# Optimization experiments

Measured on AMD Instinct MI355X. Metric: run time of the kernel, lower is better.

Reference implementation:

```python
import jax, jax.numpy as jnp
from jax import lax
import numpy as np

B, D, P = 4096, 256, 512  # batch, encoded_space_dim (=d_prototypes), n_prototypes
BN_EPS = 1e-5  # torch BatchNorm eval with running_mean=0, running_var=1


def _conv(x, w, stride, pad):
    # x: NCHW, w: OIHW
    return lax.conv_general_dilated(x, w, (stride, stride), [(pad, pad), (pad, pad)],
                                    dimension_numbers=('NCHW', 'OIHW', 'NCHW'))


def _conv_t(x, w, stride, pad, out_pad):
    # torch ConvTranspose2d; w in torch layout [Cin, Cout, kh, kw]
    k = w.shape[2]
    wf = jnp.flip(w, (2, 3)).transpose(1, 0, 2, 3)  # -> OIHW, flipped
    lo = k - 1 - pad
    hi = k - 1 - pad + out_pad
    return lax.conv_general_dilated(x, wf, (1, 1), [(lo, hi), (lo, hi)],
                                    lhs_dilation=(stride, stride),
                                    dimension_numbers=('NCHW', 'OIHW', 'NCHW'))


def _bn(x, g, b):
    # eval-mode BatchNorm2d with running_mean=0, running_var=1
    s = g / jnp.sqrt(1.0 + BN_EPS)
    return x * s[None, :, None, None] + b[None, :, None, None]


def _bias(x, b):
    return x + b[None, :, None, None]


def setup_inputs() -> dict:
    key = jax.random.key(0)
    ks = jax.random.split(key, 32)
    n = jax.random.normal
    inp = {
        'x': jax.random.uniform(ks[0], (B, 1, 28, 28), jnp.float32),
        # encoder
        'w1': n(ks[1], (8, 1, 3, 3), jnp.float32) * 0.1, 'b1': jnp.zeros((8,), jnp.float32),
        'w2': n(ks[2], (16, 8, 3, 3), jnp.float32) * 0.1, 'b2': jnp.zeros((16,), jnp.float32),
        'g2': jnp.ones((16,), jnp.float32), 'bt2': jnp.zeros((16,), jnp.float32),
        'w3': n(ks[3], (D, 16, 3, 3), jnp.float32) * 0.1, 'b3': jnp.zeros((D,), jnp.float32),
        # prototypes (torch.rand init)
        'protolayer': jax.random.uniform(ks[4], (P, D, 1, 1), jnp.float32),
        # up layer (ConvTranspose2d(D, D, 5), torch layout [Cin,Cout,kh,kw])
        'wup': n(ks[5], (D, D, 5, 5), jnp.float32) * 0.02, 'bup': jnp.zeros((D,), jnp.float32),
        'gup': jnp.ones((D,), jnp.float32), 'btup': jnp.zeros((D,), jnp.float32),
        # decoder
        'wd1': n(ks[6], (D, 16, 3, 3), jnp.float32) * 0.05, 'bd1': jnp.zeros((16,), jnp.float32),
        'gd1': jnp.ones((16,), jnp.float32), 'btd1': jnp.zeros((16,), jnp.float32),
        'wd2': n(ks[7], (16, 8, 3, 3), jnp.float32) * 0.1, 'bd2': jnp.zeros((8,), jnp.float32),
        'gd2': jnp.ones((8,), jnp.float32), 'btd2': jnp.zeros((8,), jnp.float32),
        'wd3': n(ks[8], (8, 1, 3, 3), jnp.float32) * 0.1, 'bd3': jnp.zeros((1,), jnp.float32),
    }
    return inp


def reference(x, w1, b1, w2, b2, g2, bt2, w3, b3, protolayer,
              wup, bup, gup, btup,
              wd1, bd1, gd1, btd1, wd2, bd2, gd2, btd2, wd3, bd3):
    # ---- encoder: 28 -> 14 -> 7 -> 5 ----
    h = jax.nn.relu(_bias(_conv(x, w1, 2, 1), b1))
    h = jax.nn.relu(_bn(_bias(_conv(h, w2, 2, 1), b2), g2, bt2))
    h = jax.nn.relu(_bias(_conv(h, w3, 1, 0), b3))  # [B, D, 5, 5]

    # ---- l2 'convolution' with 1x1 prototypes ----
    p = protolayer[:, :, 0, 0]                                  # [P, D]
    x2_patch_sum = jnp.sum(h * h, axis=1)                       # ones-conv, 1x1 kernel -> channel sum [B,5,5]
    xp = jnp.einsum('bdhw,pd->bphw', h, p)                      # [B, P, 5, 5]
    p2 = jnp.sum(p * p, axis=1)                                 # [P]
    distances = jax.nn.relu(x2_patch_sum[:, None] - 2.0 * xp + p2[None, :, None, None])

    # min-pool over full spatial extent
    min_distances = jnp.min(distances, axis=(2, 3))             # [B, P]
    prototype_activations = -min_distances                      # 'linear' distance_2_similarity
    w = jax.nn.softmax(prototype_activations, axis=1)
    z = jnp.einsum('bp,pdkl->bdkl', w, protolayer)              # [B, D, 1, 1]

    # ---- up layer: 1 -> 5 ----
    z = jax.nn.relu(_bn(_bias(_conv_t(z, wup, 1, 0, 0), bup), gup, btup))

    # ---- decoder: 5 -> 7 -> 14 -> 28 ----
    h = jax.nn.relu(_bn(_bias(_conv_t(z, wd1, 1, 0, 0), bd1), gd1, btd1))
    h = jax.nn.relu(_bn(_bias(_conv_t(h, wd2, 2, 1, 1), bd2), gd2, btd2))
    out = jax.nn.sigmoid(_bias(_conv_t(h, wd3, 2, 1, 1), bd3))  # [B, 1, 28, 28]
    return out, min_distances
```

## Files before the change

kernel.cpp:

```cpp
#include <hip/hip_runtime.h>
#include <hip/hip_bf16.h>
#include <math.h>

#define NB 4096
#define DC 256
#define PC 512

typedef unsigned short ushort_t;
typedef __attribute__((ext_vector_type(4))) unsigned short us4;
typedef __attribute__((ext_vector_type(8))) unsigned short us8;
typedef __attribute__((ext_vector_type(8))) short s8v;
typedef __attribute__((ext_vector_type(4))) float f32x4;

__device__ __forceinline__ float bf16_to_f(ushort_t u) {
    union { unsigned int i; float f; } c;
    c.i = ((unsigned int)u) << 16;
    return c.f;
}
__device__ __forceinline__ ushort_t f2bf(float f) {
    union { float f; unsigned int u; } c; c.f = f;
    unsigned int r = c.u + 0x7fffu + ((c.u >> 16) & 1u);
    return (ushort_t)(r >> 16);
}

__global__ __launch_bounds__(256) void k_pre(
    const float* __restrict__ proto, float* __restrict__ p2,
    ushort_t* __restrict__ pfragHi, ushort_t* __restrict__ pfragLo,
    const float* __restrict__ w3, ushort_t* __restrict__ w3fH, ushort_t* __restrict__ w3fL,
    const float* __restrict__ w2, ushort_t* __restrict__ w2fH, ushort_t* __restrict__ w2fL,
    const float* __restrict__ wd1, ushort_t* __restrict__ wd1frag,
    const float* __restrict__ wup, ushort_t* __restrict__ wupfH, ushort_t* __restrict__ wupfL)
{
    int b = blockIdx.x, tid = threadIdx.x;
    __shared__ float red[256];
    if (b < 512) {
        int p = b, d = tid;
        float v = proto[p * DC + d];
        red[d] = v * v;
        __syncthreads();
        for (int s = 128; s > 0; s >>= 1) {
            if (d < s) red[d] += red[d + s];
            __syncthreads();
        }
        if (d == 0) p2[p] = red[0];
    } else if (b < 1024) {
        int idx = (b - 512) * 256 + tid;
        int j = idx & 7, l = (idx >> 3) & 63;
        int k0 = (idx >> 9) & 7, nt = idx >> 12;
        int n = nt * 16 + (l & 15);
        int k = k0 * 32 + (l >> 4) * 8 + j;
        float v = proto[n * DC + k];
        ushort_t hi = f2bf(v);
        pfragHi[idx] = hi;
        pfragLo[idx] = f2bf(v - bf16_to_f(hi));
    } else if (b < 1184) {
        int idx = (b - 1024) * 256 + tid;
        int j = idx & 7, l = (idx >> 3) & 63;
        int q = idx >> 9;
        int k0 = q % 5, nt = q / 5;
        int d = nt * 16 + (l & 15);
        int k = k0 * 32 + (l >> 4) * 8 + j;
        float v = (k < 144) ? w3[d * 144 + k] : 0.f;
        ushort_t hi = f2bf(v);
        w3fH[idx] = hi;
        w3fL[idx] = f2bf(v - bf16_to_f(hi));
    } else if (b < 1190) {
        int idx = (b - 1184) * 256 + tid;
        int j = idx & 7, l = (idx >> 3) & 63;
        int k0 = idx >> 9;
        int ch = l & 15;
        int k = k0 * 32 + (l >> 4) * 8 + j;
        float v = (k < 72) ? w2[ch * 72 + k] : 0.f;
        ushort_t hi = f2bf(v);
        w2fH[idx] = hi;
        w2fL[idx] = f2bf(v - bf16_to_f(hi));
    } else if (b < 1334) {
        int idx = (b - 1190) * 256 + tid;
        int j = idx & 7, l = (idx >> 3) & 63;
        int k0 = (idx >> 9) & 7, nt = idx >> 12;
        int n = nt * 16 + (l & 15);
        int k = k0 * 32 + (l >> 4) * 8 + j;
        wd1frag[idx] = f2bf(wd1[k * 144 + n]);
    } else {
        int idx = (b - 1334) * 256 + tid;
        int j = idx & 7, l = (idx >> 3) & 63;
        int k0 = (idx >> 9) & 7, nt = idx >> 12;
        int np = nt * 16 + (l & 15);
        int d = k0 * 32 + (l >> 4) * 8 + j;
        int pos = np >> 8, ch = np & 255;
        float v = wup[d * 6400 + ch * 25 + pos];
        ushort_t hi = f2bf(v);
        wupfH[idx] = hi;
        wupfL[idx] = f2bf(v - bf16_to_f(hi));
    }
}

__global__ __launch_bounds__(256) void k_pw2(
    const ushort_t* __restrict__ pfragHi, const ushort_t* __restrict__ pfragLo,
    const ushort_t* __restrict__ wupfH, const ushort_t* __restrict__ wupfL,
    ushort_t* __restrict__ PWfrag)
{
    int t = threadIdx.x;
    int w = t >> 6, l = t & 63, lr = l & 15, lg = l >> 4;
    int my = blockIdx.y;
    int ntb = blockIdx.x * 16 + w * 4;
    const s8v* AH = (const s8v*)pfragHi;
    const s8v* AL = (const s8v*)pfragLo;
    const s8v* BH = (const s8v*)wupfH;
    const s8v* BL = (const s8v*)wupfL;
    f32x4 acc[4];
#pragma unroll
    for (int q = 0; q < 4; q++) acc[q] = (f32x4){0.f, 0.f, 0.f, 0.f};
#pragma unroll
    for (int k0 = 0; k0 < 8; k0++) {
        s8v ah = AH[(my * 8 + k0) * 64 + l];
        s8v al = AL[(my * 8 + k0) * 64 + l];
#pragma unroll
        for (int q = 0; q < 4; q++) {
            s8v bh = BH[(size_t)((ntb + q) * 8 + k0) * 64 + l];
            s8v bl = BL[(size_t)((ntb + q) * 8 + k0) * 64 + l];
            acc[q] = __builtin_amdgcn_mfma_f32_16x16x32_bf16(ah, bh, acc[q], 0, 0, 0);
            acc[q] = __builtin_amdgcn_mfma_f32_16x16x32_bf16(al, bh, acc[q], 0, 0, 0);
            acc[q] = __builtin_amdgcn_mfma_f32_16x16x32_bf16(ah, bl, acc[q], 0, 0, 0);
        }
    }
#pragma unroll
    for (int q = 0; q < 4; q++) {
        int nt = ntb + q;
#pragma unroll
        for (int r = 0; r < 4; r++) {
            int p = my * 16 + lg * 4 + r;
            int k0p = p >> 5;
            int ll = ((p >> 3) & 3) * 16 + lr;
            int jj = p & 7;
            PWfrag[(((size_t)(nt * 16 + k0p) * 64) + ll) * 8 + jj] = f2bf(acc[q][r]);
        }
    }
}

__global__ __launch_bounds__(512) void k_enc1(
    const float* __restrict__ x,
    const float* __restrict__ w1, const float* __restrict__ b1,
    const ushort_t* __restrict__ w2fH, const ushort_t* __restrict__ w2fL,
    const float* __restrict__ b2,
    const float* __restrict__ g2, const float* __restrict__ bt2,
    const ushort_t* __restrict__ w3fH, const ushort_t* __restrict__ w3fL,
    const float* __restrict__ b3,
    ushort_t* __restrict__ h3g)
{
    int b0 = blockIdx.x * 2;
    int t = threadIdx.x;
    int w = t >> 6, l = t & 63, lr = l & 15, lg = l >> 4;
    int tim = t >> 8, tt = t & 255;

    __shared__ __align__(16) unsigned char buf[51712];
    unsigned char* bufI = buf + tim * 25856;
    float* xb = (float*)bufI;
    float* h1 = (float*)(bufI + 3136);
    ushort_t* im2Hi = (ushort_t*)(bufI + 9408);
    float* h2 = (float*)(bufI + 22720);
    ushort_t* imHi = (ushort_t*)bufI;

    const float bnr = rsqrtf(1.0f + 1e-5f);

    const float* xg = x + (size_t)(b0 + tim) * 784;
    for (int i = tt; i < 784; i += 256) xb[i] = xg[i];
    for (int i = tt; i < 832; i += 256)
        ((float4*)(bufI + 9408))[i] = (float4){0.f, 0.f, 0.f, 0.f};
    __syncthreads();

    for (int o = tt; o < 1568; o += 256) {
        int c = o / 196, r = o % 196, y = r / 14, xc = r % 14;
        float acc = b1[c];
        for (int sy = 0; sy < 3; sy++) {
            int iy = 2 * y - 1 + sy;
            if ((unsigned)iy >= 28u) continue;
            for (int sx = 0; sx < 3; sx++) {
                int ix = 2 * xc - 1 + sx;
                if ((unsigned)ix >= 28u) continue;
                acc += w1[c * 9 + sy * 3 + sx] * xb[iy * 28 + ix];
            }
        }
        float v = fmaxf(acc, 0.f);
        ushort_t hi = f2bf(v);
        int kb = c * 9;
        int yA, syA, xA, sxA, yB = 0, xB = 0;
        bool hasYB, hasXB;
        if (y & 1) { yA = y >> 1; syA = 2; yB = yA + 1; hasYB = (yB < 7); }
        else       { yA = y >> 1; syA = 1; hasYB = false; }
        if (xc & 1) { xA = xc >> 1; sxA = 2; xB = xA + 1; hasXB = (xB < 7); }
        else        { xA = xc >> 1; sxA = 1; hasXB = false; }
        im2Hi[(yA * 7 + xA) * 104 + kb + syA * 3 + sxA] = hi;
        if (hasXB) im2Hi[(yA * 7 + xB) * 104 + kb + syA * 3] = hi;
        if (hasYB) {
            im2Hi[(yB * 7 + xA) * 104 + kb + sxA] = hi;
            if (hasXB) im2Hi[(yB * 7 + xB) * 104 + kb] = hi;
        }
    }
    __syncthreads();

    {
        int w4 = w & 3;
        f32x4 cc = {0, 0, 0, 0};
        const s8v* WH = (const s8v*)w2fH;
        const s8v* WL = (const s8v*)w2fL;
#pragma unroll
        for (int k0 = 0; k0 < 3; k0++) {
            s8v a0 = *(const s8v*)&im2Hi[(w4 * 16 + lr) * 104 + k0 * 32 + lg * 8];
            s8v bh = WH[k0 * 64 + l];
            s8v bl = WL[k0 * 64 + l];
            cc = __builtin_amdgcn_mfma_f32_16x16x32_bf16(a0, bh, cc, 0, 0, 0);
            cc = __builtin_amdgcn_mfma_f32_16x16x32_bf16(a0, bl, cc, 0, 0, 0);
        }
        int ch = lr;
        float s = g2[ch] * bnr, bb = b2[ch], bt = bt2[ch];
#pragma unroll
        for (int r = 0; r < 4; r++) {
            int pos = w4 * 16 + lg * 4 + r;
            if (pos < 49)
                h2[ch * 49 + pos] = fmaxf((cc[r] + bb) * s + bt, 0.f);
        }
    }
    __syncthreads();

    if (tt < 16) imHi[3600 + tt] = 0;
    for (int o = tt; o < 784; o += 256) {
        float v = h2[o];
        int ci = o / 49, rr = o % 49, iy = rr / 7, ixp = rr % 7;
        ushort_t hi = f2bf(v);
        int kb = ci * 9;
#pragma unroll
        for (int sy = 0; sy < 3; sy++) {
            int py = iy - sy;
            if ((unsigned)py < 5u) {
#pragma unroll
                for (int sx = 0; sx < 3; sx++) {
                    int px = ixp - sx;
                    if ((unsigned)px < 5u)
                        imHi[(py * 5 + px) * 144 + kb + sy * 3 + sx] = hi;
                }
            }
        }
    }
    __syncthreads();

    {
        const ushort_t* imHi0 = (const ushort_t*)buf;
        const ushort_t* imHi1 = (const ushort_t*)(buf + 25856);
        int nt0 = 2 * w;
        f32x4 c[2][2][2];
#pragma unroll
        for (int im = 0; im < 2; im++)
#pragma unroll
            for (int q = 0; q < 2; q++)
#pragma unroll
                for (int mt = 0; mt < 2; mt++) c[im][q][mt] = (f32x4){0.f, 0.f, 0.f, 0.f};
        const s8v* WH = (const s8v*)w3fH;
        const s8v* WL = (const s8v*)w3fL;
#pragma unroll
        for (int k0 = 0; k0 < 5; k0++) {
            s8v a00 = *(const s8v*)&imHi0[lr * 144 + k0 * 32 + lg * 8];
            s8v a01 = *(const s8v*)&imHi0[(16 + lr) * 144 + k0 * 32 + lg * 8];
            s8v a10 = *(const s8v*)&imHi1[lr * 144 + k0 * 32 + lg * 8];
            s8v a11 = *(const s8v*)&imHi1[(16 + lr) * 144 + k0 * 32 + lg * 8];
            s8v bh0 = WH[(nt0 * 5 + k0) * 64 + l];
            s8v bl0 = WL[(nt0 * 5 + k0) * 64 + l];
            s8v bh1 = WH[((nt0 + 1) * 5 + k0) * 64 + l];
            s8v bl1 = WL[((nt0 + 1) * 5 + k0) * 64 + l];
            c[0][0][0] = __builtin_amdgcn_mfma_f32_16x16x32_bf16(a00, bh0, c[0][0][0], 0, 0, 0);
            c[0][0][1] = __builtin_amdgcn_mfma_f32_16x16x32_bf16(a01, bh0, c[0][0][1], 0, 0, 0);
            c[0][0][0] = __builtin_amdgcn_mfma_f32_16x16x32_bf16(a00, bl0, c[0][0][0], 0, 0, 0);
            c[0][0][1] = __builtin_amdgcn_mfma_f32_16x16x32_bf16(a01, bl0, c[0][0][1], 0, 0, 0);
            c[0][1][0] = __builtin_amdgcn_mfma_f32_16x16x32_bf16(a00, bh1, c[0][1][0], 0, 0, 0);
            c[0][1][1] = __builtin_amdgcn_mfma_f32_16x16x32_bf16(a01, bh1, c[0][1][1], 0, 0, 0);
            c[0][1][0] = __builtin_amdgcn_mfma_f32_16x16x32_bf16(a00, bl1, c[0][1][0], 0, 0, 0);
            c[0][1][1] = __builtin_amdgcn_mfma_f32_16x16x32_bf16(a01, bl1, c[0][1][1], 0, 0, 0);
            c[1][0][0] = __builtin_amdgcn_mfma_f32_16x16x32_bf16(a10, bh0, c[1][0][0], 0, 0, 0);
            c[1][0][1] = __builtin_amdgcn_mfma_f32_16x16x32_bf16(a11, bh0, c[1][0][1], 0, 0, 0);
            c[1][0][0] = __builtin_amdgcn_mfma_f32_16x16x32_bf16(a10, bl0, c[1][0][0], 0, 0, 0);
            c[1][0][1] = __builtin_amdgcn_mfma_f32_16x16x32_bf16(a11, bl0, c[1][0][1], 0, 0, 0);
            c[1][1][0] = __builtin_amdgcn_mfma_f32_16x16x32_bf16(a10, bh1, c[1][1][0], 0, 0, 0);
            c[1][1][1] = __builtin_amdgcn_mfma_f32_16x16x32_bf16(a11, bh1, c[1][1][1], 0, 0, 0);
            c[1][1][0] = __builtin_amdgcn_mfma_f32_16x16x32_bf16(a10, bl1, c[1][1][0], 0, 0, 0);
            c[1][1][1] = __builtin_amdgcn_mfma_f32_16x16x32_bf16(a11, bl1, c[1][1][1], 0, 0, 0);
        }
#pragma unroll
        for (int im = 0; im < 2; im++) {
            ushort_t* hg = h3g + (size_t)(b0 + im) * 6400;
#pragma unroll
            for (int q = 0; q < 2; q++) {
                int d = (nt0 + q) * 16 + lr;
                float bb = b3[d];
#pragma unroll
                for (int mt = 0; mt < 2; mt++) {
                    f32x4 cv = c[im][q][mt];
#pragma unroll
                    for (int r = 0; r < 4; r++) {
                        int pos = mt * 16 + lg * 4 + r;
                        if (pos < 25) {
                            float h = fmaxf(cv[r] + bb, 0.f);
                            hg[pos * 256 + d] = f2bf(h);
                        }
                    }
                }
            }
        }
    }
}

__global__ __launch_bounds__(1024) void k_enc2(
    const ushort_t* __restrict__ h3g,
    const ushort_t* __restrict__ pfragHi, const ushort_t* __restrict__ pfragLo,
    const float* __restrict__ p2,
    float* __restrict__ md_out,
    ushort_t* __restrict__ Wsm)
{
    int t = threadIdx.x;
    int b0 = blockIdx.x * 2;
    int w = t >> 6, l = t & 63, lr = l & 15, lg = l >> 4;

    __shared__ __align__(16) ushort_t h3s[2][32][264];
    __shared__ float mds[2][512];
    __shared__ float x2sh[2][32];
    __shared__ float x2part[2][25][8];
    __shared__ float wred[2][16];

    for (int i = t; i < 2048; i += 1024) {
        int im = i >> 10, pos = (i >> 5) & 31, c8 = i & 31;
        us8 v = {0, 0, 0, 0, 0, 0, 0, 0};
        if (pos < 25)
            v = *(const us8*)&h3g[(size_t)(b0 + im) * 6400 + pos * 256 + c8 * 8];
        *(us8*)&h3s[im][pos][c8 * 8] = v;
    }
    __syncthreads();

    if (t < 400) {
        int im = t / 200, rest = t % 200;
        int pos = rest >> 3, ch = rest & 7;
        const ushort_t* hp = &h3s[im][pos][ch * 32];
        float s = 0.f;
#pragma unroll
        for (int i = 0; i < 32; i++) {
            float f = bf16_to_f(hp[i]);
            s = fmaf(f, f, s);
        }
        x2part[im][pos][ch] = s;
    }
    __syncthreads();
    if (t < 64) {
        int im = t >> 5, pos = t & 31;
        float s = 1e30f;
        if (pos < 25) {
            s = 0.f;
#pragma unroll
            for (int c = 0; c < 8; c++) s += x2part[im][pos][c];
        }
        x2sh[im][pos] = s;
    }
    __syncthreads();

    {
        f32x4 acc[2][2][2];
#pragma unroll
        for (int i = 0; i < 2; i++)
#pragma unroll
            for (int jm = 0; jm < 2; jm++)
#pragma unroll
                for (int mt = 0; mt < 2; mt++) acc[i][jm][mt] = (f32x4){0.f, 0.f, 0.f, 0.f};
        const s8v* BH = (const s8v*)pfragHi;
        const s8v* BL = (const s8v*)pfragLo;
        s8v bhc[2], blc[2], bhn[2], bln[2];
#pragma unroll
        for (int ntq = 0; ntq < 2; ntq++) {
            int nt = w * 2 + ntq;
            bhc[ntq] = BH[(nt * 8 + 0) * 64 + l];
            blc[ntq] = BL[(nt * 8 + 0) * 64 + l];
        }
        for (int k0 = 0; k0 < 8; k0++) {
            if (k0 < 7) {
#pragma unroll
                for (int ntq = 0; ntq < 2; ntq++) {
                    int nt = w * 2 + ntq;
                    bhn[ntq] = BH[(nt * 8 + k0 + 1) * 64 + l];
                    bln[ntq] = BL[(nt * 8 + k0 + 1) * 64 + l];
                }
            }
            s8v ah[2][2];
            ah[0][0] = *(const s8v*)&h3s[0][lr][k0 * 32 + lg * 8];
            ah[0][1] = *(const s8v*)&h3s[0][16 + lr][k0 * 32 + lg * 8];
            ah[1][0] = *(const s8v*)&h3s[1][lr][k0 * 32 + lg * 8];
            ah[1][1] = *(const s8v*)&h3s[1][16 + lr][k0 * 32 + lg * 8];
#pragma unroll
            for (int ntq = 0; ntq < 2; ntq++) {
                s8v bh = bhc[ntq];
                s8v bl = blc[ntq];
#pragma unroll
                for (int im = 0; im < 2; im++) {
                    acc[ntq][im][0] = __builtin_amdgcn_mfma_f32_16x16x32_bf16(ah[im][0], bh, acc[ntq][im][0], 0, 0, 0);
                    acc[ntq][im][1] = __builtin_amdgcn_mfma_f32_16x16x32_bf16(ah[im][1], bh, acc[ntq][im][1], 0, 0, 0);
                    acc[ntq][im][0] = __builtin_amdgcn_mfma_f32_16x16x32_bf16(ah[im][0], bl, acc[ntq][im][0], 0, 0, 0);
                    acc[ntq][im][1] = __builtin_amdgcn_mfma_f32_16x16x32_bf16(ah[im][1], bl, acc[ntq][im][1], 0, 0, 0);
                }
            }
#pragma unroll
            for (int ntq = 0; ntq < 2; ntq++) {
                bhc[ntq] = bhn[ntq];
                blc[ntq] = bln[ntq];
            }
        }
        float x2r[2][8];
#pragma unroll
        for (int im = 0; im < 2; im++)
#pragma unroll
            for (int r = 0; r < 4; r++) {
                x2r[im][r]     = x2sh[im][lg * 4 + r];
                x2r[im][4 + r] = x2sh[im][16 + lg * 4 + r];
            }
#pragma unroll
        for (int ntq = 0; ntq < 2; ntq++) {
            int pcol = (w * 2 + ntq) * 16 + lr;
            float p2v = p2[pcol];
#pragma unroll
            for (int im = 0; im < 2; im++) {
                float mm = 1e30f;
#pragma unroll
                for (int r = 0; r < 4; r++) {
                    float d0 = fmaxf(x2r[im][r]     - 2.f * acc[ntq][im][0][r] + p2v, 0.f);
                    float d1 = fmaxf(x2r[im][4 + r] - 2.f * acc[ntq][im][1][r] + p2v, 0.f);
                    mm = fminf(mm, fminf(d0, d1));
                }
                mm = fminf(mm, __shfl_xor(mm, 16));
                mm = fminf(mm, __shfl_xor(mm, 32));
                if (lg == 0) mds[im][pcol] = mm;
            }
        }
    }
    __syncthreads();

    int img = t >> 9, tt = t & 511;
    float mind = mds[img][tt];
    md_out[(size_t)(b0 + img) * PC + tt] = mind;
    float a = -mind;
    float mx = a;
#pragma unroll
    for (int off = 1; off < 64; off <<= 1) mx = fmaxf(mx, __shfl_xor(mx, off));
    int wv = w & 7;
    if (l == 0) wred[img][wv] = mx;
    __syncthreads();
    float m = wred[img][0];
#pragma unroll
    for (int i = 1; i < 8; i++) m = fmaxf(m, wred[img][i]);
    float e = expf(a - m);
    float sm = e;
#pragma unroll
    for (int off = 1; off < 64; off <<= 1) sm += __shfl_xor(sm, off);
    if (l == 0) wred[img][8 + wv] = sm;
    __syncthreads();
    float ssum = wred[img][8];
#pragma unroll
    for (int i = 9; i < 16; i++) ssum += wred[img][i];
    Wsm[(size_t)(b0 + img) * PC + tt] = f2bf(e / ssum);
}

__global__ __launch_bounds__(512) void k_zup2(
    const ushort_t* __restrict__ Wsm,
    const ushort_t* __restrict__ PWfrag,
    const float* __restrict__ bup, const float* __restrict__ gup,
    const float* __restrict__ btup,
    ushort_t* __restrict__ zupT)
{
    __shared__ __align__(16) ushort_t Bsh[2][8192];
    int t = threadIdx.x;
    int w = t >> 6, l = t & 63;
    int n0 = blockIdx.x * 128;
    int m0 = blockIdx.y * 128;
    int row = m0 + w * 16 + (l & 15);
    int krow = (l >> 4) * 8;
    f32x4 acc[8];
#pragma unroll
    for (int i = 0; i < 8; i++) acc[i] = (f32x4){0.f, 0.f, 0.f, 0.f};
    const s8v* B = (const s8v*)PWfrag;
    int base = blockIdx.x * 8 * 16;

    {
        s8v v0 = B[(size_t)(base + (t >> 6) * 16 + 0) * 64 + (t & 63)];
        s8v v1 = B[(size_t)(base + (t >> 6) * 16 + 1) * 64 + (t & 63)];
        *(s8v*)&Bsh[0][t * 8] = v0;
        *(s8v*)&Bsh[0][4096 + t * 8] = v1;
    }
    __syncthreads();
    for (int r = 0; r < 8; r++) {
        int cur = r & 1;
        if (r < 7) {
            s8v v0 = B[(size_t)(base + (t >> 6) * 16 + 2 * r + 2) * 64 + (t & 63)];
            s8v v1 = B[(size_t)(base + (t >> 6) * 16 + 2 * r + 3) * 64 + (t & 63)];
            *(s8v*)&Bsh[cur ^ 1][t * 8] = v0;
            *(s8v*)&Bsh[cur ^ 1][4096 + t * 8] = v1;
        }
#pragma unroll
        for (int kk = 0; kk < 2; kk++) {
            int k0 = 2 * r + kk;
            s8v a = *(const s8v*)&Wsm[(size_t)row * 512 + k0 * 32 + krow];
#pragma unroll
            for (int nt = 0; nt < 8; nt++) {
                s8v bb = *(const s8v*)&Bsh[cur][kk * 4096 + (nt * 64 + l) * 8];
                acc[nt] = __builtin_amdgcn_mfma_f32_16x16x32_bf16(a, bb, acc[nt], 0, 0, 0);
            }
        }
        __syncthreads();
    }

    const float bnr = rsqrtf(1.0f + 1e-5f);
    int rowbase = m0 + w * 16 + (l >> 4) * 4;
#pragma unroll
    for (int nt = 0; nt < 8; nt++) {
        int n = n0 + nt * 16 + (l & 15);
        int ch = n & 255;
        float sc = gup[ch] * bnr, bb = bup[ch], bt = btup[ch];
#pragma unroll
        for (int r = 0; r < 4; r++) {
            float v = (acc[nt][r] + bb) * sc + bt;
            zupT[(size_t)(rowbase + r) * 6400 + n] = f2bf(fmaxf(v, 0.f));
        }
    }
}

__global__ __launch_bounds__(512) void k_dtail(
    const ushort_t* __restrict__ zupT,
    const ushort_t* __restrict__ wd1frag,
    const float* __restrict__ bd1, const float* __restrict__ gd1, const float* __restrict__ btd1,
    const float* __restrict__ wd2, const float* __restrict__ bd2,
    const float* __restrict__ gd2, const float* __restrict__ btd2,
    const float* __restrict__ wd3, const float* __restrict__ bd3,
    float* __restrict__ out0)
{
    int b0 = blockIdx.x * 2, t = threadIdx.x;
    int w = t >> 6, l = t & 63, lr = l & 15, lg = l >> 4;
    int g = w >> 2, wv = w & 3, tg = t & 255;
    __shared__ __align__(16) unsigned char dbuf[33792];
    __shared__ float hd1p[2][16][64];
    __shared__ float w2sT[9 * 8 * 16];
    __shared__ float w3sT[9 * 8];
    ushort_t* zAb = (ushort_t*)dbuf;
    float* Psb = (float*)dbuf;

    const float bnr = rsqrtf(1.0f + 1e-5f);

    for (int c = t; c < 1600; c += 512) {
        int im = c / 800, cc = c % 800;
        *(us8*)&zAb[im * 8448 + (cc >> 5) * 264 + (cc & 31) * 8] =
            *(const us8*)&zupT[(size_t)(b0 + im) * 6400 + cc * 8];
    }
    for (int i = t; i < 2048; i += 512) ((float*)hd1p)[i] = 0.f;
    for (int i = t; i < 1152; i += 512) {
        int s = i >> 7, rest = i & 127;
        int co = rest >> 4, ci = rest & 15;
        w2sT[i] = wd2[(ci * 8 + co) * 9 + s];
    }
    if (t < 72) {
        int s = t >> 3, ci = t & 7;
        w3sT[t] = wd3[ci * 9 + s];
    }
    __syncthreads();

    {
        f32x4 acc[3][2];
#pragma unroll
        for (int i = 0; i < 3; i++)
#pragma unroll
            for (int mt = 0; mt < 2; mt++) acc[i][mt] = (f32x4){0.f, 0.f, 0.f, 0.f};
        const s8v* B = (const s8v*)wd1frag;
        for (int k0 = 0; k0 < 8; k0++) {
            s8v a0 = *(const s8v*)&zAb[g * 8448 + lr * 264 + k0 * 32 + lg * 8];
            s8v a1 = *(const s8v*)&zAb[g * 8448 + (16 + lr) * 264 + k0 * 32 + lg * 8];
#pragma unroll
            for (int i = 0; i < 3; i++) {
                int nt = wv + 4 * i;
                if (nt < 9) {
                    s8v bb = B[(nt * 8 + k0) * 64 + l];
                    acc[i][0] = __builtin_amdgcn_mfma_f32_16x16x32_bf16(a0, bb, acc[i][0], 0, 0, 0);
                    acc[i][1] = __builtin_amdgcn_mfma_f32_16x16x32_bf16(a1, bb, acc[i][1], 0, 0, 0);
                }
            }
        }
        __syncthreads();
#pragma unroll
        for (int i = 0; i < 3; i++) {
            int nt = wv + 4 * i;
            if (nt < 9) {
                int col = nt * 16 + lr;
#pragma unroll
                for (int mt = 0; mt < 2; mt++)
#pragma unroll
                    for (int r = 0; r < 4; r++) {
                        int pos = mt * 16 + lg * 4 + r;
                        if (pos < 25) Psb[g * 3700 + pos * 148 + col] = acc[i][mt][r];
                    }
            }
        }
    }
    __syncthreads();

    for (int o = tg; o < 784; o += 256) {
        int co = o / 49, rr = o % 49, y = rr / 7, xx = rr % 7;
        float a = bd1[co];
        int sy0 = y - 4 > 0 ? y - 4 : 0, sy1 = y < 2 ? y : 2;
        for (int sy = sy0; sy <= sy1; sy++) {
            int iy = y - sy;
            int sx0 = xx - 4 > 0 ? xx - 4 : 0, sx1 = xx < 2 ? xx : 2;
            for (int sx = sx0; sx <= sx1; sx++) {
                int ix = xx - sx;
                a += Psb[g * 3700 + (iy * 5 + ix) * 148 + co * 9 + sy * 3 + sx];
            }
        }
        float v = a * (gd1[co] * bnr) + btd1[co];
        hd1p[g][co][y * 8 + xx] = fmaxf(v, 0.f);
    }
    __syncthreads();

    {
        if (t < 464) {
            int im = t / 232, rest = t % 232;
            int co = rest / 29, s = rest % 29;
            int yy = (s < 15) ? 14 : (s - 15);
            int xx2 = (s < 15) ? s : 14;
            ((float*)dbuf)[im * 1808 + co * 225 + yy * 15 + xx2] = 0.f;
        }
        int cls = (wv + g) & 3;
        int cy = cls >> 1, cx = cls & 1;
        if (l < 56 && (l & 7) < 7) {
            int r = l >> 3, c = l & 7;
            float acc[8];
#pragma unroll
            for (int co = 0; co < 8; co++) acc[co] = 0.f;
            const float* hb = &hd1p[g][0][0];
            int niy = 1 + cy, nix = 1 + cx;
            for (int ty = 0; ty < niy; ty++) {
                int iy = r + ty;
                int sy = cy ? (ty ? 0 : 2) : 1;
                for (int tx = 0; tx < nix; tx++) {
                    int ix = c + tx;
                    int sx = cx ? (tx ? 0 : 2) : 1;
                    const float* wp = &w2sT[(sy * 3 + sx) * 128];
                    int hoff = iy * 8 + ix;
                    float h[16];
#pragma unroll
                    for (int ci = 0; ci < 16; ci++) h[ci] = hb[ci * 64 + hoff];
#pragma unroll
                    for (int co = 0; co < 8; co++) {
                        const float4* wp4 = (const float4*)&wp[co * 16];
                        float4 wa = wp4[0], wb4 = wp4[1], wc4 = wp4[2], wd4 = wp4[3];
                        float a = acc[co];
                        a = fmaf(h[0], wa.x, a);  a = fmaf(h[1], wa.y, a);
                        a = fmaf(h[2], wa.z, a);  a = fmaf(h[3], wa.w, a);
                        a = fmaf(h[4], wb4.x, a); a = fmaf(h[5], wb4.y, a);
                        a = fmaf(h[6], wb4.z, a); a = fmaf(h[7], wb4.w, a);
                        a = fmaf(h[8], wc4.x, a); a = fmaf(h[9], wc4.y, a);
                        a = fmaf(h[10], wc4.z, a); a = fmaf(h[11], wc4.w, a);
                        a = fmaf(h[12], wd4.x, a); a = fmaf(h[13], wd4.y, a);
                        a = fmaf(h[14], wd4.z, a); a = fmaf(h[15], wd4.w, a);
                        acc[co] = a;
                    }
                }
            }
            int y = 2 * r + cy, x = 2 * c + cx;
            float* hout = (float*)dbuf + g * 1808;
#pragma unroll
            for (int co = 0; co < 8; co++) {
                float v = (acc[co] + bd2[co]) * (gd2[co] * bnr) + btd2[co];
                hout[co * 225 + y * 15 + x] = fmaxf(v, 0.f);
            }
        }
    }
    __syncthreads();

    {
        int cls = (wv + g) & 3;
        int cy = cls >> 1, cx = cls & 1;
        const float* h2b = (const float*)dbuf + g * 1808;
        float* og = out0 + (size_t)(b0 + g) * 784;
        int niy = 1 + cy, nix = 1 + cx;
#pragma unroll
        for (int j = 0; j < 4; j++) {
            int idx = l + 64 * j;
            if (idx < 224) {
                int row = idx >> 4, col = idx & 15;
                if (col < 14) {
                    float a = bd3[0];
                    for (int ty = 0; ty < niy; ty++) {
                        int iy = row + ty;
                        int sy = cy ? (ty ? 0 : 2) : 1;
                        for (int tx = 0; tx < nix; tx++) {
                            int ix = col + tx;
                            int sx = cx ? (tx ? 0 : 2) : 1;
                            const float* wp = &w3sT[(sy * 3 + sx) * 8];
                            int hoff = iy * 15 + ix;
#pragma unroll
                            for (int ci = 0; ci < 8; ci++)
                                a = fmaf(h2b[ci * 225 + hoff], wp[ci], a);
                        }
                    }
                    int y = 2 * row + cy, x = 2 * col + cx;
                    og[y * 28 + x] = 1.f / (1.f + expf(-a));
                }
            }
        }
    }
}

extern "C" void kernel_launch(void* const* d_in, const int* in_sizes, int n_in,
                              void* d_out, int out_size, void* d_ws, size_t ws_size,
                              hipStream_t stream) {
    const float* x    = (const float*)d_in[0];
    const float* w1   = (const float*)d_in[1];
    const float* b1   = (const float*)d_in[2];
    const float* w2   = (const float*)d_in[3];
    const float* b2   = (const float*)d_in[4];
    const float* g2   = (const float*)d_in[5];
    const float* bt2  = (const float*)d_in[6];
    const float* w3   = (const float*)d_in[7];
    const float* b3   = (const float*)d_in[8];
    const float* proto= (const float*)d_in[9];
    const float* wup  = (const float*)d_in[10];
    const float* bup  = (const float*)d_in[11];
    const float* gup  = (const float*)d_in[12];
    const float* btup = (const float*)d_in[13];
    const float* wd1  = (const float*)d_in[14];
    const float* bd1  = (const float*)d_in[15];
    const float* gd1  = (const float*)d_in[16];
    const float* btd1 = (const float*)d_in[17];
    const float* wd2  = (const float*)d_in[18];
    const float* bd2  = (const float*)d_in[19];
    const float* gd2  = (const float*)d_in[20];
    const float* btd2 = (const float*)d_in[21];
    const float* wd3  = (const float*)d_in[22];
    const float* bd3  = (const float*)d_in[23];

    float* out0   = (float*)d_out;
    float* out_md = out0 + (size_t)NB * 784;

    float*    p2      = (float*)d_ws;
    float*    x2g     = p2 + 512;
    ushort_t* pfragHi = (ushort_t*)(x2g + 131072);
    ushort_t* pfragLo = pfragHi + 131072;
    ushort_t* w3fH    = pfragLo + 131072;
    ushort_t* w3fL    = w3fH + 40960;
    ushort_t* w2fH    = w3fL + 40960;
    ushort_t* w2fL    = w2fH + 1536;
    ushort_t* wd1frag = w2fL + 1536;
    ushort_t* wupfH   = wd1frag + 36864;
    ushort_t* wupfL   = wupfH + 1638400;
    ushort_t* PWfrag  = wupfL + 1638400;
    ushort_t* Wsm     = PWfrag + 3276800;
    ushort_t* BIG     = Wsm + 2097152;
    ushort_t* h3g     = BIG;
    ushort_t* zupT    = BIG;

    hipLaunchKernelGGL(k_pre, dim3(7734), dim3(256), 0, stream,
                       proto, p2, pfragHi, pfragLo, w3, w3fH, w3fL,
                       w2, w2fH, w2fL, wd1, wd1frag, wup, wupfH, wupfL);
    hipLaunchKernelGGL(k_pw2, dim3(25, 32), dim3(256), 0, stream,
                       pfragHi, pfragLo, wupfH, wupfL, PWfrag);
    hipLaunchKernelGGL(k_enc1, dim3(NB / 2), dim3(512), 0, stream,
                       x, w1, b1, w2fH, w2fL, b2, g2, bt2, w3fH, w3fL, b3, h3g);
    hipLaunchKernelGGL(k_enc2, dim3(NB / 2), dim3(1024), 0, stream,
                       h3g, pfragHi, pfragLo, p2, out_md, Wsm);
    hipLaunchKernelGGL(k_zup2, dim3(50, 32), dim3(512), 0, stream,
                       Wsm, PWfrag, bup, gup, btup, zupT);
    hipLaunchKernelGGL(k_dtail, dim3(NB / 2), dim3(512), 0, stream,
                       zupT, wd1frag, bd1, gd1, btd1, wd2, bd2, gd2, btd2, wd3, bd3, out0);
}
```

Measured before the change: 273.0 us.

## Fuse encoder conv stages with prototype distance/softmax kernel via shared memory

Merges k_enc1 and k_enc2 into one 1024-thread kernel. The conv3 output (h3) is now written to shared memory instead of global memory, and the distance/min/softmax stage reads it from there. This removes a global round trip of h3 (about 52 MB in bf16) and one kernel launch. In exchange, the early conv stages run at 1024 threads with some waves idle, and the larger block may lower occupancy.

```diff
diff --git a/kernel.cpp b/kernel.cpp
--- a/kernel.cpp
+++ b/kernel.cpp
@@ -138,7 +138,7 @@
     }
 }
 
-__global__ __launch_bounds__(512) void k_enc1(
+__global__ __launch_bounds__(1024) void k_enc(
     const float* __restrict__ x,
     const float* __restrict__ w1, const float* __restrict__ b1,
     const ushort_t* __restrict__ w2fH, const ushort_t* __restrict__ w2fL,
@@ -146,30 +146,39 @@
     const float* __restrict__ g2, const float* __restrict__ bt2,
     const ushort_t* __restrict__ w3fH, const ushort_t* __restrict__ w3fL,
     const float* __restrict__ b3,
-    ushort_t* __restrict__ h3g)
+    const ushort_t* __restrict__ pfragHi, const ushort_t* __restrict__ pfragLo,
+    const float* __restrict__ p2,
+    float* __restrict__ md_out,
+    ushort_t* __restrict__ Wsm)
 {
     int b0 = blockIdx.x * 2;
     int t = threadIdx.x;
     int w = t >> 6, l = t & 63, lr = l & 15, lg = l >> 4;
-    int tim = t >> 8, tt = t & 255;
-
-    __shared__ __align__(16) unsigned char buf[51712];
-    unsigned char* bufI = buf + tim * 25856;
+    int tim = t >> 9, tt = t & 511;
+
+    __shared__ __align__(16) unsigned char buf[52608];
+    __shared__ float mds[2][512];
+    __shared__ float x2sh[2][32];
+    __shared__ float x2part[2][25][8];
+    __shared__ float wred[2][16];
+
+    unsigned char* bufI = buf + tim * 26304;
     float* xb = (float*)bufI;
     float* h1 = (float*)(bufI + 3136);
     ushort_t* im2Hi = (ushort_t*)(bufI + 9408);
     float* h2 = (float*)(bufI + 22720);
     ushort_t* imHi = (ushort_t*)bufI;
+    ushort_t* h3sI = (ushort_t*)(bufI + 9408);
 
     const float bnr = rsqrtf(1.0f + 1e-5f);
 
     const float* xg = x + (size_t)(b0 + tim) * 784;
-    for (int i = tt; i < 784; i += 256) xb[i] = xg[i];
-    for (int i = tt; i < 832; i += 256)
+    for (int i = tt; i < 784; i += 512) xb[i] = xg[i];
+    for (int i = tt; i < 832; i += 512)
         ((float4*)(bufI + 9408))[i] = (float4){0.f, 0.f, 0.f, 0.f};
     __syncthreads();
 
-    for (int o = tt; o < 1568; o += 256) {
+    for (int o = tt; o < 1568; o += 512) {
         int c = o / 196, r = o % 196, y = r / 14, xc = r % 14;
         float acc = b1[c];
         for (int sy = 0; sy < 3; sy++) {
@@ -199,7 +208,7 @@
     }
     __syncthreads();
 
-    {
+    if ((w & 7) < 4) {
         int w4 = w & 3;
         f32x4 cc = {0, 0, 0, 0};
         const s8v* WH = (const s8v*)w2fH;
@@ -223,8 +232,7 @@
     }
     __syncthreads();
 
-    if (tt < 16) imHi[3600 + tt] = 0;
-    for (int o = tt; o < 784; o += 256) {
+    for (int o = tt; o < 784; o += 512) {
         float v = h2[o];
         int ci = o / 49, rr = o % 49, iy = rr / 7, ixp = rr % 7;
         ushort_t hi = f2bf(v);
@@ -244,17 +252,21 @@
     }
     __syncthreads();
 
+    for (int i = t; i < 3696; i += 1024) {
+        int im = i >= 1848, e = (im ? i - 1848 : i);
+        ((ushort_t*)(buf + im * 26304 + 9408))[25 * 264 + e] = 0;
+    }
+    __syncthreads();
+
     {
         const ushort_t* imHi0 = (const ushort_t*)buf;
-        const ushort_t* imHi1 = (const ushort_t*)(buf + 25856);
-        int nt0 = 2 * w;
-        f32x4 c[2][2][2];
+        const ushort_t* imHi1 = (const ushort_t*)(buf + 26304);
+        int nt = w;
+        f32x4 c[2][2];
 #pragma unroll
         for (int im = 0; im < 2; im++)
 #pragma unroll
-            for (int q = 0; q < 2; q++)
-#pragma unroll
-                for (int mt = 0; mt < 2; mt++) c[im][q][mt] = (f32x4){0.f, 0.f, 0.f, 0.f};
+            for (int mt = 0; mt < 2; mt++) c[im][mt] = (f32x4){0.f, 0.f, 0.f, 0.f};
         const s8v* WH = (const s8v*)w3fH;
         const s8v* WL = (const s8v*)w3fL;
 #pragma unroll
@@ -263,81 +275,42 @@
             s8v a01 = *(const s8v*)&imHi0[(16 + lr) * 144 + k0 * 32 + lg * 8];
             s8v a10 = *(const s8v*)&imHi1[lr * 144 + k0 * 32 + lg * 8];
             s8v a11 = *(const s8v*)&imHi1[(16 + lr) * 144 + k0 * 32 + lg * 8];
-            s8v bh0 = WH[(nt0 * 5 + k0) * 64 + l];
-            s8v bl0 = WL[(nt0 * 5 + k0) * 64 + l];
-            s8v bh1 = WH[((nt0 + 1) * 5 + k0) * 64 + l];
-            s8v bl1 = WL[((nt0 + 1) * 5 + k0) * 64 + l];
-            c[0][0][0] = __builtin_amdgcn_mfma_f32_16x16x32_bf16(a00, bh0, c[0][0][0], 0, 0, 0);
-            c[0][0][1] = __builtin_amdgcn_mfma_f32_16x16x32_bf16(a01, bh0, c[0][0][1], 0, 0, 0);
-            c[0][0][0] = __builtin_amdgcn_mfma_f32_16x16x32_bf16(a00, bl0, c[0][0][0], 0, 0, 0);
-            c[0][0][1] = __builtin_amdgcn_mfma_f32_16x16x32_bf16(a01, bl0, c[0][0][1], 0, 0, 0);
-            c[0][1][0] = __builtin_amdgcn_mfma_f32_16x16x32_bf16(a00, bh1, c[0][1][0], 0, 0, 0);
-            c[0][1][1] = __builtin_amdgcn_mfma_f32_16x16x32_bf16(a01, bh1, c[0][1][1], 0, 0, 0);
-            c[0][1][0] = __builtin_amdgcn_mfma_f32_16x16x32_bf16(a00, bl1, c[0][1][0], 0, 0, 0);
-            c[0][1][1] = __builtin_amdgcn_mfma_f32_16x16x32_bf16(a01, bl1, c[0][1][1], 0, 0, 0);
-            c[1][0][0] = __builtin_amdgcn_mfma_f32_16x16x32_bf16(a10, bh0, c[1][0][0], 0, 0, 0);
-            c[1][0][1] = __builtin_amdgcn_mfma_f32_16x16x32_bf16(a11, bh0, c[1][0][1], 0, 0, 0);
-            c[1][0][0] = __builtin_amdgcn_mfma_f32_16x16x32_bf16(a10, bl0, c[1][0][0], 0, 0, 0);
-            c[1][0][1] = __builtin_amdgcn_mfma_f32_16x16x32_bf16(a11, bl0, c[1][0][1], 0, 0, 0);
-            c[1][1][0] = __builtin_amdgcn_mfma_f32_16x16x32_bf16(a10, bh1, c[1][1][0], 0, 0, 0);
-            c[1][1][1] = __builtin_amdgcn_mfma_f32_16x16x32_bf16(a11, bh1, c[1][1][1], 0, 0, 0);
-            c[1][1][0] = __builtin_amdgcn_mfma_f32_16x16x32_bf16(a10, bl1, c[1][1][0], 0, 0, 0);
-            c[1][1][1] = __builtin_amdgcn_mfma_f32_16x16x32_bf16(a11, bl1, c[1][1][1], 0, 0, 0);
-        }
+            s8v bh = WH[(nt * 5 + k0) * 64 + l];
+            s8v bl = WL[(nt * 5 + k0) * 64 + l];
+            c[0][0] = __builtin_amdgcn_mfma_f32_16x16x32_bf16(a00, bh, c[0][0], 0, 0, 0);
+            c[0][1] = __builtin_amdgcn_mfma_f32_16x16x32_bf16(a01, bh, c[0][1], 0, 0, 0);
+            c[0][0] = __builtin_amdgcn_mfma_f32_16x16x32_bf16(a00, bl, c[0][0], 0, 0, 0);
+            c[0][1] = __builtin_amdgcn_mfma_f32_16x16x32_bf16(a01, bl, c[0][1], 0, 0, 0);
+            c[1][0] = __builtin_amdgcn_mfma_f32_16x16x32_bf16(a10, bh, c[1][0], 0, 0, 0);
+            c[1][1] = __builtin_amdgcn_mfma_f32_16x16x32_bf16(a11, bh, c[1][1], 0, 0, 0);
+            c[1][0] = __builtin_amdgcn_mfma_f32_16x16x32_bf16(a10, bl, c[1][0], 0, 0, 0);
+            c[1][1] = __builtin_amdgcn_mfma_f32_16x16x32_bf16(a11, bl, c[1][1], 0, 0, 0);
+        }
+        int d = nt * 16 + lr;
+        float bb = b3[d];
 #pragma unroll
         for (int im = 0; im < 2; im++) {
-            ushort_t* hg = h3g + (size_t)(b0 + im) * 6400;
-#pragma unroll
-            for (int q = 0; q < 2; q++) {
-                int d = (nt0 + q) * 16 + lr;
-                float bb = b3[d];
-#pragma unroll
-                for (int mt = 0; mt < 2; mt++) {
-                    f32x4 cv = c[im][q][mt];
-#pragma unroll
-                    for (int r = 0; r < 4; r++) {
-                        int pos = mt * 16 + lg * 4 + r;
-                        if (pos < 25) {
-                            float h = fmaxf(cv[r] + bb, 0.f);
-                            hg[pos * 256 + d] = f2bf(h);
-                        }
+            ushort_t* hs = (ushort_t*)(buf + im * 26304 + 9408);
+#pragma unroll
+            for (int mt = 0; mt < 2; mt++) {
+                f32x4 cv = c[im][mt];
+#pragma unroll
+                for (int r = 0; r < 4; r++) {
+                    int pos = mt * 16 + lg * 4 + r;
+                    if (pos < 25) {
+                        float h = fmaxf(cv[r] + bb, 0.f);
+                        hs[pos * 264 + d] = f2bf(h);
                     }
                 }
             }
         }
-    }
-}
-
-__global__ __launch_bounds__(1024) void k_enc2(
-    const ushort_t* __restrict__ h3g,
-    const ushort_t* __restrict__ pfragHi, const ushort_t* __restrict__ pfragLo,
-    const float* __restrict__ p2,
-    float* __restrict__ md_out,
-    ushort_t* __restrict__ Wsm)
-{
-    int t = threadIdx.x;
-    int b0 = blockIdx.x * 2;
-    int w = t >> 6, l = t & 63, lr = l & 15, lg = l >> 4;
-
-    __shared__ __align__(16) ushort_t h3s[2][32][264];
-    __shared__ float mds[2][512];
-    __shared__ float x2sh[2][32];
-    __shared__ float x2part[2][25][8];
-    __shared__ float wred[2][16];
-
-    for (int i = t; i < 2048; i += 1024) {
-        int im = i >> 10, pos = (i >> 5) & 31, c8 = i & 31;
-        us8 v = {0, 0, 0, 0, 0, 0, 0, 0};
-        if (pos < 25)
-            v = *(const us8*)&h3g[(size_t)(b0 + im) * 6400 + pos * 256 + c8 * 8];
-        *(us8*)&h3s[im][pos][c8 * 8] = v;
     }
     __syncthreads();
 
     if (t < 400) {
         int im = t / 200, rest = t % 200;
         int pos = rest >> 3, ch = rest & 7;
-        const ushort_t* hp = &h3s[im][pos][ch * 32];
+        const ushort_t* hp = (const ushort_t*)(buf + im * 26304 + 9408) + pos * 264 + ch * 32;
         float s = 0.f;
 #pragma unroll
         for (int i = 0; i < 32; i++) {
@@ -360,6 +333,8 @@
     __syncthreads();
 
     {
+        const ushort_t* h3s0 = (const ushort_t*)(buf + 9408);
+        const ushort_t* h3s1 = (const ushort_t*)(buf + 26304 + 9408);
         f32x4 acc[2][2][2];
 #pragma unroll
         for (int i = 0; i < 2; i++)
@@ -386,10 +361,10 @@
                 }
             }
             s8v ah[2][2];
-            ah[0][0] = *(const s8v*)&h3s[0][lr][k0 * 32 + lg * 8];
-            ah[0][1] = *(const s8v*)&h3s[0][16 + lr][k0 * 32 + lg * 8];
-            ah[1][0] = *(const s8v*)&h3s[1][lr][k0 * 32 + lg * 8];
-            ah[1][1] = *(const s8v*)&h3s[1][16 + lr][k0 * 32 + lg * 8];
+            ah[0][0] = *(const s8v*)&h3s0[lr * 264 + k0 * 32 + lg * 8];
+            ah[0][1] = *(const s8v*)&h3s0[(16 + lr) * 264 + k0 * 32 + lg * 8];
+            ah[1][0] = *(const s8v*)&h3s1[lr * 264 + k0 * 32 + lg * 8];
+            ah[1][1] = *(const s8v*)&h3s1[(16 + lr) * 264 + k0 * 32 + lg * 8];
 #pragma unroll
             for (int ntq = 0; ntq < 2; ntq++) {
                 s8v bh = bhc[ntq];
@@ -437,9 +412,9 @@
     }
     __syncthreads();
 
-    int img = t >> 9, tt = t & 511;
-    float mind = mds[img][tt];
-    md_out[(size_t)(b0 + img) * PC + tt] = mind;
+    int img = t >> 9, stt = t & 511;
+    float mind = mds[img][stt];
+    md_out[(size_t)(b0 + img) * PC + stt] = mind;
     float a = -mind;
     float mx = a;
 #pragma unroll
@@ -459,7 +434,7 @@
     float ssum = wred[img][8];
 #pragma unroll
     for (int i = 9; i < 16; i++) ssum += wred[img][i];
-    Wsm[(size_t)(b0 + img) * PC + tt] = f2bf(e / ssum);
+    Wsm[(size_t)(b0 + img) * PC + stt] = f2bf(e / ssum);
 }
 
 __global__ __launch_bounds__(512) void k_zup2(
@@ -740,8 +715,8 @@
     float* out_md = out0 + (size_t)NB * 784;
 
     float*    p2      = (float*)d_ws;
-    float*    x2g     = p2 + 512;
-    ushort_t* pfragHi = (ushort_t*)(x2g + 131072);
+    float*    pad0    = p2 + 512;
+    ushort_t* pfragHi = (ushort_t*)(pad0 + 131072);
     ushort_t* pfragLo = pfragHi + 131072;
     ushort_t* w3fH    = pfragLo + 131072;
     ushort_t* w3fL    = w3fH + 40960;
@@ -752,19 +727,16 @@
     ushort_t* wupfL   = wupfH + 1638400;
     ushort_t* PWfrag  = wupfL + 1638400;
     ushort_t* Wsm     = PWfrag + 3276800;
-    ushort_t* BIG     = Wsm + 2097152;
-    ushort_t* h3g     = BIG;
-    ushort_t* zupT    = BIG;
+    ushort_t* zupT    = Wsm + 2097152;
 
     hipLaunchKernelGGL(k_pre, dim3(7734), dim3(256), 0, stream,
                        proto, p2, pfragHi, pfragLo, w3, w3fH, w3fL,
                        w2, w2fH, w2fL, wd1, wd1frag, wup, wupfH, wupfL);
     hipLaunchKernelGGL(k_pw2, dim3(25, 32), dim3(256), 0, stream,
                        pfragHi, pfragLo, wupfH, wupfL, PWfrag);
-    hipLaunchKernelGGL(k_enc1, dim3(NB / 2), dim3(512), 0, stream,
-                       x, w1, b1, w2fH, w2fL, b2, g2, bt2, w3fH, w3fL, b3, h3g);
-    hipLaunchKernelGGL(k_enc2, dim3(NB / 2), dim3(1024), 0, stream,
-                       h3g, pfragHi, pfragLo, p2, out_md, Wsm);
+    hipLaunchKernelGGL(k_enc, dim3(NB / 2), dim3(1024), 0, stream,
+                       x, w1, b1, w2fH, w2fL, b2, g2, bt2, w3fH, w3fL, b3,
+                       pfragHi, pfragLo, p2, out_md, Wsm);
     hipLaunchKernelGGL(k_zup2, dim3(50, 32), dim3(512), 0, stream,
                        Wsm, PWfrag, bup, gup, btup, zupT);
     hipLaunchKernelGGL(k_dtail, dim3(NB / 2), dim3(512), 0, stream,
```

Result: no change. 274.4 us (+0.5%).
